# Optimization experiments

Hardware: AMD Instinct MI355X
Metric: run time of the kernel (lower is better)

The kernel has to match this reference:

```python
import jax, jax.numpy as jnp
import numpy as np

B, L, D = 4, 2048, 1024
DK, H = 64, 16
DFF = 4 * D
MASK_FILL = -2**15 + 1  # -32767, matches masked_fill value in source


def setup_inputs() -> dict:
    key = jax.random.key(0)
    ks = jax.random.split(key, 16)
    s = lambda fan_in: 1.0 / np.sqrt(fan_in)
    inp = {
        "x": jax.random.normal(ks[0], (B, L, D), dtype=jnp.float32),
        "maskPAD": jax.random.randint(ks[1], (B, L, L), 0, 2, dtype=jnp.int32),
        # attention projections (torch Linear layout: [out, in])
        "WQ_w": jax.random.uniform(ks[2], (H * DK, D), jnp.float32, -s(D), s(D)),
        "WQ_b": jnp.zeros((H * DK,), jnp.float32),
        "WK_w": jax.random.uniform(ks[3], (H * DK, D), jnp.float32, -s(D), s(D)),
        "WK_b": jnp.zeros((H * DK,), jnp.float32),
        "WV_w": jax.random.uniform(ks[4], (H * DK, D), jnp.float32, -s(D), s(D)),
        "WV_b": jnp.zeros((H * DK,), jnp.float32),
        "WO_w": jax.random.uniform(ks[5], (D, H * DK), jnp.float32, -s(H * DK), s(H * DK)),
        "WO_b": jnp.zeros((D,), jnp.float32),
        # FFN (pre-LN inside the FFN block)
        "ln_g": jnp.ones((D,), jnp.float32),
        "ln_b": jnp.zeros((D,), jnp.float32),
        "W1_w": jax.random.uniform(ks[6], (DFF, D), jnp.float32, -s(D), s(D)),
        "W1_b": jnp.zeros((DFF,), jnp.float32),
        "W2_w": jax.random.uniform(ks[7], (D, DFF), jnp.float32, -s(DFF), s(DFF)),
        "W2_b": jnp.zeros((D,), jnp.float32),
    }
    return inp


def _layernorm(x, g, b, eps=1e-5):
    mu = jnp.mean(x, axis=-1, keepdims=True)
    var = jnp.var(x, axis=-1, keepdims=True)
    return (x - mu) * jax.lax.rsqrt(var + eps) * g + b


def reference(x, maskPAD, WQ_w, WQ_b, WK_w, WK_b, WV_w, WV_b, WO_w, WO_b,
              ln_g, ln_b, W1_w, W1_b, W2_w, W2_b):
    # --- SelfAttention_PostLN (dropout = identity at eval) ---
    q = (jnp.einsum('bld,ed->ble', x, WQ_w) + WQ_b).reshape(B, L, H, DK).transpose(0, 2, 1, 3)
    k = (jnp.einsum('bld,ed->ble', x, WK_w) + WK_b).reshape(B, L, H, DK).transpose(0, 2, 1, 3)
    v = (jnp.einsum('bld,ed->ble', x, WV_w) + WV_b).reshape(B, L, H, DK).transpose(0, 2, 1, 3)
    scores = jnp.einsum('bhqd,bhkd->bhqk', q, k) / np.sqrt(DK).astype(np.float32)
    scores = jnp.where((maskPAD == 0)[:, None, :, :], jnp.float32(MASK_FILL), scores)
    alpha = jax.nn.softmax(scores, axis=-1)
    z = jnp.einsum('bhqk,bhkd->bhqd', alpha, v)  # [B,H,L,DK]
    z = z.transpose(0, 2, 1, 3).reshape(B, L, H * DK)
    z = jnp.einsum('ble,de->bld', z, WO_w) + WO_b
    # --- FFN_PreLN ---
    r = x + z                                    # residual 1 (dropout identity)
    h = _layernorm(r, ln_g, ln_b)
    h = jax.nn.relu(jnp.einsum('bld,fd->blf', h, W1_w) + W1_b)
    h = jnp.einsum('blf,df->bld', h, W2_w) + W2_b
    return r + h
```

## Files before the change

### kernel.cpp

```cpp
#include <hip/hip_runtime.h>

#define BD      4
#define LSEQ    2048
#define DMODEL  1024
#define HHEADS  16
#define DKK     64
#define DFFN    4096
#define MROWS   (BD*LSEQ)
#define QKVS    3072

typedef float  f32x4  __attribute__((ext_vector_type(4)));
typedef float  f32x16 __attribute__((ext_vector_type(16)));
typedef __bf16 bf16x8 __attribute__((ext_vector_type(8)));
typedef unsigned short u16x8 __attribute__((ext_vector_type(8)));
typedef unsigned int   u32x4 __attribute__((ext_vector_type(4)));

__device__ inline unsigned short f2bf(float x) {
    union { float f; unsigned u; } c; c.f = x;
    unsigned r = c.u + 0x7FFFu + ((c.u >> 16) & 1u);
    return (unsigned short)(r >> 16);
}

__global__ void cast_bf16_k(const float* __restrict__ in,
                            unsigned short* __restrict__ out, long n) {
    long i = ((long)blockIdx.x * blockDim.x + threadIdx.x) * 4;
    long stride = (long)gridDim.x * blockDim.x * 4;
    for (; i < n; i += stride) {
        float4 v = *(const float4*)(in + i);
        ushort4 o;
        o.x = f2bf(v.x); o.y = f2bf(v.y); o.z = f2bf(v.z); o.w = f2bf(v.w);
        *(ushort4*)(out + i) = o;
    }
}

__global__ __launch_bounds__(256) void maskbits_k(const int* __restrict__ m,
                                                  unsigned long long* __restrict__ bits) {
    const long gw = ((long)blockIdx.x * blockDim.x + threadIdx.x) >> 6;
    const int lane = threadIdx.x & 63;
    const int b   = (int)(gw >> 16);
    const int rem = (int)gw & 65535;
    const int q = rem >> 5, kt = rem & 31;
    const int v = m[((size_t)(b*LSEQ + q))*LSEQ + kt*64 + lane];
    const unsigned long long bal = __ballot(v != 0);
    if (lane == 0) bits[((size_t)(b*32 + kt))*LSEQ + q] = bal;
}

__device__ inline void gload16(const void* g, void* l) {
    __builtin_amdgcn_global_load_lds(
        (const __attribute__((address_space(1))) void*)g,
        (__attribute__((address_space(3))) void*)l, 16, 0, 0);
}

#define BAR() { __builtin_amdgcn_sched_barrier(0); __builtin_amdgcn_s_barrier(); __builtin_amdgcn_sched_barrier(0); }

#define STAGE(XSEL, XPTR, h, tau, s)                                              \
  { const unsigned short* gs0 = (XPTR) + (size_t)((h)*128 + wid*8 + srow) * K + (tau)*64 + schk*8; \
    gload16(gs0, (void*)&sm[(s)][(XSEL)][(((h)*128 + wid*8)*64)]);                 \
    gload16(gs0 + (size_t)64*K, (void*)&sm[(s)][(XSEL)][(((h)*128 + 64 + wid*8)*64)]); }

#define LDA(dst, s, mi, kk) dst = *(const bf16x8*)(&sm[(s)][0][(wr*128 + (mi)*16 + r0)*64 + ((((kk)*4 + g) ^ (r0 & 7)) << 3)]);
#define LDB(dst, s, nj, kk) dst = *(const bf16x8*)(&sm[(s)][1][(wc*64  + (nj)*16 + r0)*64 + ((((kk)*4 + g) ^ (r0 & 7)) << 3)]);

#define PHASE_MFMA(q)                                                                                   \
    __builtin_amdgcn_s_setprio(1);                                                                      \
    _Pragma("unroll")                                                                                   \
    for (int nj = 0; nj < 4; ++nj) {                                                                    \
        acc[2*(q)][nj]   = __builtin_amdgcn_mfma_f32_16x16x32_bf16(af00, bq[nj][0], acc[2*(q)][nj],   0,0,0); \
        acc[2*(q)][nj]   = __builtin_amdgcn_mfma_f32_16x16x32_bf16(af01, bq[nj][1], acc[2*(q)][nj],   0,0,0); \
        acc[2*(q)+1][nj] = __builtin_amdgcn_mfma_f32_16x16x32_bf16(af10, bq[nj][0], acc[2*(q)+1][nj], 0,0,0); \
        acc[2*(q)+1][nj] = __builtin_amdgcn_mfma_f32_16x16x32_bf16(af11, bq[nj][1], acc[2*(q)+1][nj], 0,0,0); \
    }                                                                                                   \
    __builtin_amdgcn_s_setprio(0);

#define KTILE(s, tau)                                                        \
  {                                                                          \
    const int tp1 = (tau) + 1, tp2 = (tau) + 2;                              \
    bf16x8 bq[4][2];                                                         \
    bf16x8 af00, af01, af10, af11;                                           \
                              \
    _Pragma("unroll") for (int nj = 0; nj < 4; ++nj) {                       \
        LDB(bq[nj][0], s, nj, 0); LDB(bq[nj][1], s, nj, 1); }                \
    LDA(af00, s, 0, 0); LDA(af01, s, 0, 1);                                  \
    LDA(af10, s, 1, 0); LDA(af11, s, 1, 1);                                  \
    if (tp1 < NTT) { STAGE(0, Ab, 0, tp1, (s)^1); }                          \
    BAR(); PHASE_MFMA(0); BAR();                                             \
                           \
    LDA(af00, s, 2, 0); LDA(af01, s, 2, 1);                                  \
    LDA(af10, s, 3, 0); LDA(af11, s, 3, 1);                                  \
    if (tp1 < NTT) { STAGE(0, Ab, 1, tp1, (s)^1); }                          \
    if (tp2 < NTT) { STAGE(1, Bb, 0, tp2, (s)); }                            \
    BAR(); PHASE_MFMA(1); BAR();                                             \
                                      \
    LDA(af00, s, 4, 0); LDA(af01, s, 4, 1);                                  \
    LDA(af10, s, 5, 0); LDA(af11, s, 5, 1);                                  \
    if (tp2 < NTT) { STAGE(1, Bb, 1, tp2, (s)); }                            \
    BAR(); PHASE_MFMA(2); BAR();                                             \
                                        \
    LDA(af00, s, 6, 0); LDA(af01, s, 6, 1);                                  \
    LDA(af10, s, 7, 0); LDA(af11, s, 7, 1);                                  \
    if (tp2 < NTT)      { asm volatile("s_waitcnt vmcnt(4)" ::: "memory"); } \
    else if (tp1 < NTT) { asm volatile("s_waitcnt vmcnt(0)" ::: "memory"); } \
    BAR(); PHASE_MFMA(3); BAR();                                             \
  }

template<int MODE, int NTT>
__global__ __launch_bounds__(512, 2) void gemm8(const unsigned short* __restrict__ A,
                                                const unsigned short* __restrict__ B,
                                                const float* __restrict__ bias,
                                                unsigned short* __restrict__ Cout,
                                                int M, int N, int K, float scaleQ)
{
    __shared__ unsigned short sm[2][2][256*64];
    const int t   = threadIdx.x;
    const int wid = t >> 6, lane = t & 63;
    const int wr  = wid >> 2, wc = wid & 3;
    const int r0  = lane & 15, g = lane >> 4;

    const int nwg = gridDim.x;
    const int bid = (blockIdx.x & 7) * (nwg >> 3) + (blockIdx.x >> 3);
    const int ntn = N >> 8;
    const int bm  = (bid / ntn) << 8, bn = (bid % ntn) << 8;

    const int srow = lane >> 3;
    const int schk = (lane & 7) ^ srow;
    const unsigned short* Ab = A + (size_t)bm * K;
    const unsigned short* Bb = B + (size_t)bn * K;

    f32x4 acc[8][4] = {};

    STAGE(1, Bb, 0, 0, 0); STAGE(1, Bb, 1, 0, 0);
    STAGE(0, Ab, 0, 0, 0); STAGE(0, Ab, 1, 0, 0);
    STAGE(1, Bb, 0, 1, 1); STAGE(1, Bb, 1, 1, 1);
    asm volatile("s_waitcnt vmcnt(4)" ::: "memory");
    BAR();

#pragma unroll 1
    for (int i2 = 0; i2 < NTT/2; ++i2) {
        const int tau = 2*i2;
        KTILE(0, tau);
        KTILE(1, tau+1);
    }

#pragma unroll
    for (int mi = 0; mi < 8; ++mi) {
        const int row0 = bm + wr*128 + mi*16 + g*4;
#pragma unroll
        for (int nj = 0; nj < 4; ++nj) {
            const int col = bn + wc*64 + nj*16 + r0;
            const float bcol = bias[col];
            const float sc = (MODE == 0) ? (col < 1024 ? scaleQ : 1.0f) : 1.0f;
#pragma unroll
            for (int rr = 0; rr < 4; ++rr) {
                float c = (acc[mi][nj][rr] + bcol) * sc;
                if (MODE == 1) c = fmaxf(c, 0.f);
                Cout[(size_t)(row0 + rr) * N + col] = f2bf(c);
            }
        }
    }
}

template<int MODE>
__global__ __launch_bounds__(256) void gemm_nt(const unsigned short* __restrict__ A,
                                               const unsigned short* __restrict__ B,
                                               const float* __restrict__ bias,
                                               const float* __restrict__ resid,
                                               void* __restrict__ Cout,
                                               int M, int N, int K, float scale)
{
    __shared__ unsigned short As[128*32];
    __shared__ unsigned short Bs[128*32];
    const int t    = threadIdx.x;
    const int w    = t >> 6, lane = t & 63;
    const int r0   = lane & 15, g = lane >> 4;
    const int wm   = (w >> 1) * 64, wn = (w & 1) * 64;
    const int bm   = blockIdx.y * 128, bn = blockIdx.x * 128;
    const int srow = t >> 2, scol = (t & 3) * 8;

    const unsigned short* Ag = A + (size_t)(bm + srow) * K + scol;
    const unsigned short* Bg = B + (size_t)(bn + srow) * K + scol;
    unsigned short* AsW = As + w * 512;
    unsigned short* BsW = Bs + w * 512;

    f32x4 acc[4][4] = {};

    for (int kt = 0; kt < K; kt += 32) {
        gload16(Ag + kt,                AsW);
        gload16(Ag + (size_t)64*K + kt, AsW + 2048);
        gload16(Bg + kt,                BsW);
        gload16(Bg + (size_t)64*K + kt, BsW + 2048);
        __syncthreads();
        bf16x8 af[4], bfr[4];
#pragma unroll
        for (int i = 0; i < 4; ++i)
            af[i] = *(const bf16x8*)(As + (wm + i*16 + r0)*32 + g*8);
#pragma unroll
        for (int j = 0; j < 4; ++j)
            bfr[j] = *(const bf16x8*)(Bs + (wn + j*16 + r0)*32 + g*8);
#pragma unroll
        for (int i = 0; i < 4; ++i)
#pragma unroll
            for (int j = 0; j < 4; ++j)
                acc[i][j] = __builtin_amdgcn_mfma_f32_16x16x32_bf16(af[i], bfr[j], acc[i][j], 0, 0, 0);
        __syncthreads();
    }

#pragma unroll
    for (int i = 0; i < 4; ++i) {
        const int row0 = bm + wm + i*16 + g*4;
#pragma unroll
        for (int j = 0; j < 4; ++j) {
            const int col = bn + wn + j*16 + r0;
            const float bcol = bias[col];
#pragma unroll
            for (int rr = 0; rr < 4; ++rr) {
                const int row = row0 + rr;
                float c = (acc[i][j][rr] + bcol) * scale;
                if (MODE == 2) {
                    ((float*)Cout)[(size_t)row * N + col] = c + resid[(size_t)row * N + col];
                } else {
                    if (MODE == 1) c = fmaxf(c, 0.f);
                    ((unsigned short*)Cout)[(size_t)row * N + col] = f2bf(c);
                }
            }
        }
    }
}

#define MFILL   (-47272.79f)
#define DEFTHR  (11.5415603f)
__global__ __launch_bounds__(256) void attn_k(
    const unsigned short* __restrict__ QKV,
    const unsigned long long* __restrict__ MBits,
    unsigned short* __restrict__ Z)
{
    __shared__ unsigned short Ks[2][64*64];
    __shared__ unsigned short Vt[64*64];
    __shared__ float Sc[4*32];

    const int t    = threadIdx.x;
    const int w    = t >> 6, lane = t & 63;
    const int q31  = lane & 31, hi = lane >> 5;

    const int bid = blockIdx.x;
    const int sw  = (bid & 7) * 128 + (bid >> 3);
    const int qt  = sw & 15, h = (sw >> 4) & 15, b = sw >> 8;
    const int qw  = qt * 128 + w * 32;

    const unsigned short* Qg = QKV + ((size_t)(b*LSEQ + qw + q31))*QKVS + h*DKK + hi*8;
    bf16x8 qf[4];
#pragma unroll
    for (int ds = 0; ds < 4; ++ds)
        qf[ds] = *(const bf16x8*)(Qg + ds*16);

    const int krow  = w*8 + (lane>>3);
    const int kchk  = (lane & 7) ^ (krow & 7);
    const unsigned short* Kg = QKV + ((size_t)(b*LSEQ))*QKVS + 1024 + h*DKK;
    const int kp   = w*8 + (lane>>3);
    const int vd0  = (lane & 7) * 8;
    const unsigned short* Vg = QKV + ((size_t)(b*LSEQ))*QKVS + 2048 + h*DKK + vd0;

    float m_r = MFILL, l_r = 0.f;
    f32x16 z0, z1;
#pragma unroll
    for (int r = 0; r < 16; ++r) { z0[r] = 0.f; z1[r] = 0.f; }

    u16x8 vA = *(const u16x8*)(Vg + (size_t)(kp*2)*QKVS);
    u16x8 vB = *(const u16x8*)(Vg + (size_t)(kp*2+1)*QKVS);
#pragma unroll
    for (int i = 0; i < 8; ++i) {
        const int d = vd0 + i;
        const int c = (kp>>2) ^ (d&7) ^ (d>>3);
        *(unsigned*)&Vt[d*64 + c*8 + 2*(kp&3)] = (unsigned)vA[i] | ((unsigned)vB[i] << 16);
    }
    gload16(Kg + (size_t)krow*QKVS      + kchk*8, &Ks[0][w*512]);
    gload16(Kg + (size_t)(32+krow)*QKVS + kchk*8, &Ks[0][w*512] + 2048);

    for (int kt = 0; kt < LSEQ/64; ++kt) {
        const int cur = kt & 1;
        __syncthreads();

        if (kt < LSEQ/64 - 1) {
            const int k0n = (kt+1)*64;
            gload16(Kg + (size_t)(k0n + krow)*QKVS      + kchk*8, &Ks[cur^1][w*512]);
            gload16(Kg + (size_t)(k0n + 32 + krow)*QKVS + kchk*8, &Ks[cur^1][w*512] + 2048);
            vA = *(const u16x8*)(Vg + (size_t)(k0n + kp*2)*QKVS);
            vB = *(const u16x8*)(Vg + (size_t)(k0n + kp*2+1)*QKVS);
        }
        const unsigned long long mw = MBits[((size_t)(b*32 + kt))*LSEQ + (qw + q31)];
        const unsigned long long sh = mw >> (hi*4);
        const unsigned md0 = (unsigned)sh, md1 = (unsigned)(sh >> 32);

        f32x16 s0, s1;
#pragma unroll
        for (int r = 0; r < 16; ++r) { s0[r] = 0.f; s1[r] = 0.f; }
        __builtin_amdgcn_s_setprio(1);
#pragma unroll
        for (int ds = 0; ds < 4; ++ds) {
            const int slot = ((ds*2 + hi) ^ (q31 & 7)) << 3;
            bf16x8 kf0 = *(const bf16x8*)(&Ks[cur][ q31     *64 + slot]);
            bf16x8 kf1 = *(const bf16x8*)(&Ks[cur][(32+q31)*64 + slot]);
            s0 = __builtin_amdgcn_mfma_f32_32x32x16_bf16(kf0, qf[ds], s0, 0, 0, 0);
            s1 = __builtin_amdgcn_mfma_f32_32x32x16_bf16(kf1, qf[ds], s1, 0, 0, 0);
        }
        __builtin_amdgcn_s_setprio(0);

#pragma unroll
        for (int r = 0; r < 16; ++r) {
            const int kb = (r & 3) + 8*(r >> 2);
            if (!((md0 >> kb) & 1)) s0[r] = MFILL;
            if (!((md1 >> kb) & 1)) s1[r] = MFILL;
        }

        float tm = fmaxf(s0[0], s1[0]);
#pragma unroll
        for (int r = 1; r < 16; ++r) tm = fmaxf(tm, fmaxf(s0[r], s1[r]));
        {
            float ta = tm, tb = tm;
            asm volatile("v_permlane32_swap_b32 %0, %1" : "+v"(ta), "+v"(tb));
            tm = fmaxf(tm, hi ? ta : tb);
        }

        if (__any(tm > m_r + DEFTHR)) {
            const float nm   = fmaxf(m_r, tm);
            const float corr = exp2f(m_r - nm);
            Sc[w*32 + q31] = corr;
            l_r *= corr;
            m_r  = nm;
#pragma unroll
            for (int r = 0; r < 16; ++r) {
                const int row = (r & 3) + 8*(r >> 2) + 4*hi;
                const float cr = Sc[w*32 + row];
                z0[r] *= cr; z1[r] *= cr;
            }
        }

#pragma unroll
        for (int r = 0; r < 16; ++r) {
            s0[r] = exp2f(s0[r] - m_r);
            s1[r] = exp2f(s1[r] - m_r);
        }
        float r4[8];
#pragma unroll
        for (int r = 0; r < 8; ++r)
            r4[r] = (s0[2*r] + s0[2*r+1]) + (s1[2*r] + s1[2*r+1]);
        float rs = ((r4[0]+r4[1]) + (r4[2]+r4[3])) + ((r4[4]+r4[5]) + (r4[6]+r4[7]));
        {
            float ra = rs, rb = rs;
            asm volatile("v_permlane32_swap_b32 %0, %1" : "+v"(ra), "+v"(rb));
            rs += hi ? ra : rb;
        }
        l_r += rs;

        bf16x8 pa[4];
#pragma unroll
        for (int half = 0; half < 2; ++half) {
#pragma unroll
            for (int sub = 0; sub < 2; ++sub) {
                const int base = sub*8;
                unsigned wa, wb, wc, wd;
                float p0 = half ? s1[base+0] : s0[base+0];
                float p1 = half ? s1[base+1] : s0[base+1];
                float p2 = half ? s1[base+2] : s0[base+2];
                float p3 = half ? s1[base+3] : s0[base+3];
                float p4 = half ? s1[base+4] : s0[base+4];
                float p5 = half ? s1[base+5] : s0[base+5];
                float p6 = half ? s1[base+6] : s0[base+6];
                float p7 = half ? s1[base+7] : s0[base+7];
                asm("v_cvt_pk_bf16_f32 %0, %1, %2" : "=v"(wa) : "v"(p0), "v"(p1));
                asm("v_cvt_pk_bf16_f32 %0, %1, %2" : "=v"(wb) : "v"(p4), "v"(p5));
                asm("v_cvt_pk_bf16_f32 %0, %1, %2" : "=v"(wc) : "v"(p2), "v"(p3));
                asm("v_cvt_pk_bf16_f32 %0, %1, %2" : "=v"(wd) : "v"(p6), "v"(p7));
                asm volatile("v_permlane32_swap_b32 %0, %1" : "+v"(wa), "+v"(wb));
                asm volatile("v_permlane32_swap_b32 %0, %1" : "+v"(wc), "+v"(wd));
                u32x4 pu; pu[0] = wa; pu[1] = wc; pu[2] = wb; pu[3] = wd;
                pa[half*2 + sub] = __builtin_bit_cast(bf16x8, pu);
            }
        }

        __builtin_amdgcn_s_setprio(1);
#pragma unroll
        for (int ks = 0; ks < 4; ++ks) {
            const int ch = ks*2 + hi;
            bf16x8 vf0 = *(const bf16x8*)(&Vt[ q31     *64 + ((ch ^ (q31&7) ^ ( q31>>3)     ) << 3)]);
            bf16x8 vf1 = *(const bf16x8*)(&Vt[(32+q31)*64 + ((ch ^ (q31&7) ^ ((32+q31)>>3)) << 3)]);
            z0 = __builtin_amdgcn_mfma_f32_32x32x16_bf16(pa[ks], vf0, z0, 0, 0, 0);
            z1 = __builtin_amdgcn_mfma_f32_32x32x16_bf16(pa[ks], vf1, z1, 0, 0, 0);
        }
        __builtin_amdgcn_s_setprio(0);

        __syncthreads();

        if (kt < LSEQ/64 - 1) {
#pragma unroll
            for (int i = 0; i < 8; ++i) {
                const int d = vd0 + i;
                const int c = (kp>>2) ^ (d&7) ^ (d>>3);
                *(unsigned*)&Vt[d*64 + c*8 + 2*(kp&3)] = (unsigned)vA[i] | ((unsigned)vB[i] << 16);
            }
        }
    }

    Sc[w*32 + q31] = l_r;
    unsigned short* Zb = Z + ((size_t)(b*LSEQ + qw))*DMODEL + h*DKK + q31;
#pragma unroll
    for (int r = 0; r < 16; ++r) {
        const int row = (r & 3) + 8*(r >> 2) + 4*hi;
        const float rl = 1.0f / Sc[w*32 + row];
        Zb[(size_t)row*DMODEL]      = f2bf(z0[r] * rl);
        Zb[(size_t)row*DMODEL + 32] = f2bf(z1[r] * rl);
    }
}

__global__ __launch_bounds__(256) void ln_k(const float* __restrict__ r,
                                            const float* __restrict__ gam,
                                            const float* __restrict__ bet,
                                            unsigned short* __restrict__ out)
{
    const int row = blockIdx.x;
    const int t = threadIdx.x;
    const float* rp = r + (size_t)row * DMODEL;
    float4 v = *(const float4*)(rp + t*4);
    float s  = v.x + v.y + v.z + v.w;
    float s2 = v.x*v.x + v.y*v.y + v.z*v.z + v.w*v.w;
#pragma unroll
    for (int off = 32; off >= 1; off >>= 1) {
        s  += __shfl_xor(s,  off);
        s2 += __shfl_xor(s2, off);
    }
    __shared__ float red[8];
    const int wv = t >> 6;
    if ((t & 63) == 0) { red[wv] = s; red[4 + wv] = s2; }
    __syncthreads();
    s  = red[0] + red[1] + red[2] + red[3];
    s2 = red[4] + red[5] + red[6] + red[7];
    const float mu   = s  * (1.f/DMODEL);
    const float var  = s2 * (1.f/DMODEL) - mu*mu;
    const float rstd = rsqrtf(var + 1e-5f);
    float4 gv = *(const float4*)(gam + t*4);
    float4 bv = *(const float4*)(bet + t*4);
    ushort4 o;
    o.x = f2bf((v.x - mu)*rstd*gv.x + bv.x);
    o.y = f2bf((v.y - mu)*rstd*gv.y + bv.y);
    o.z = f2bf((v.z - mu)*rstd*gv.z + bv.z);
    o.w = f2bf((v.w - mu)*rstd*gv.w + bv.w);
    *(ushort4*)(out + (size_t)row * DMODEL + t*4) = o;
}

extern "C" void kernel_launch(void* const* d_in, const int* in_sizes, int n_in,
                              void* d_out, int out_size, void* d_ws, size_t ws_size,
                              hipStream_t stream)
{
    const float* x    = (const float*)d_in[0];
    const int*   mask = (const int*)  d_in[1];
    const float* WQ_w = (const float*)d_in[2];
    const float* WQ_b = (const float*)d_in[3];
    const float* WK_w = (const float*)d_in[4];
    const float* WK_b = (const float*)d_in[5];
    const float* WV_w = (const float*)d_in[6];
    const float* WV_b = (const float*)d_in[7];
    const float* WO_w = (const float*)d_in[8];
    const float* WO_b = (const float*)d_in[9];
    const float* ln_g = (const float*)d_in[10];
    const float* ln_b = (const float*)d_in[11];
    const float* W1_w = (const float*)d_in[12];
    const float* W1_b = (const float*)d_in[13];
    const float* W2_w = (const float*)d_in[14];
    const float* W2_b = (const float*)d_in[15];
    float* out = (float*)d_out;

    char* w = (char*)d_ws;
    const size_t MB = 1024*1024;
    unsigned short* qkv  = (unsigned short*)(w + 0*MB);
    unsigned short* Zb   = (unsigned short*)(w + 48*MB);
    unsigned short* xb   = (unsigned short*)(w + 64*MB);
    float*          rb   = (float*)         (w + 80*MB);
    unsigned short* wqkv = (unsigned short*)(w + 112*MB);
    unsigned short* wob  = (unsigned short*)(w + 118*MB);
    unsigned short* w1b  = (unsigned short*)(w + 120*MB);
    unsigned short* w2b  = (unsigned short*)(w + 128*MB);
    unsigned long long* mbits = (unsigned long long*)(w + 136*MB);
    float* bqkv = (float*)(w + 48*MB);
    unsigned short* hln  = xb;
    unsigned short* hmid = (unsigned short*)(w + 0*MB);

    cast_bf16_k<<<2048, 256, 0, stream>>>(x,    xb,   (long)MROWS*DMODEL);
    cast_bf16_k<<<512,  256, 0, stream>>>(WQ_w, wqkv,                 (long)DMODEL*DMODEL);
    cast_bf16_k<<<512,  256, 0, stream>>>(WK_w, wqkv + 1024*1024,     (long)DMODEL*DMODEL);
    cast_bf16_k<<<512,  256, 0, stream>>>(WV_w, wqkv + 2*1024*1024,   (long)DMODEL*DMODEL);
    cast_bf16_k<<<512,  256, 0, stream>>>(WO_w, wob,  (long)DMODEL*DMODEL);
    cast_bf16_k<<<2048, 256, 0, stream>>>(W1_w, w1b,  (long)DFFN*DMODEL);
    cast_bf16_k<<<2048, 256, 0, stream>>>(W2_w, w2b,  (long)DMODEL*DFFN);
    maskbits_k<<<65536, 256, 0, stream>>>(mask, mbits);
    hipMemcpyAsync(bqkv,        WQ_b, 1024*sizeof(float), hipMemcpyDeviceToDevice, stream);
    hipMemcpyAsync(bqkv + 1024, WK_b, 1024*sizeof(float), hipMemcpyDeviceToDevice, stream);
    hipMemcpyAsync(bqkv + 2048, WV_b, 1024*sizeof(float), hipMemcpyDeviceToDevice, stream);

    gemm8<0, 16><<<dim3(384), dim3(512), 0, stream>>>(xb, wqkv, bqkv, qkv,
                                                      MROWS, QKVS, DMODEL, 0.18033688f);
    attn_k<<<dim3(1024), dim3(256), 0, stream>>>(qkv, mbits, Zb);
    gemm_nt<2><<<dim3(8, 64), dim3(256), 0, stream>>>(Zb, wob, WO_b, x, rb, MROWS, DMODEL, DMODEL, 1.0f);
    ln_k<<<MROWS, 256, 0, stream>>>(rb, ln_g, ln_b, hln);
    gemm8<1, 16><<<dim3(512), dim3(512), 0, stream>>>(hln, w1b, W1_b, hmid,
                                                      MROWS, DFFN, DMODEL, 1.0f);
    gemm_nt<2><<<dim3(8, 64), dim3(256), 0, stream>>>(hmid, w2b, W2_b, rb, out, MROWS, DMODEL, DFFN, 1.0f);
}
```

Baseline: 519.4 us.

## Add 256x128 GEMM variant, restructure attention pipelining, fuse bias concat

```diff
diff --git a/kernel.cpp b/kernel.cpp
--- a/kernel.cpp
+++ b/kernel.cpp
@@ -31,6 +31,12 @@
         o.x = f2bf(v.x); o.y = f2bf(v.y); o.z = f2bf(v.z); o.w = f2bf(v.w);
         *(ushort4*)(out + i) = o;
     }
+}
+
+__global__ void concat3_k(const float* __restrict__ a, const float* __restrict__ b,
+                          const float* __restrict__ c, float* __restrict__ o) {
+    int i = blockIdx.x * 256 + threadIdx.x;
+    if (i < 1024) { o[i] = a[i]; o[1024 + i] = b[i]; o[2048 + i] = c[i]; }
 }
 
 __global__ __launch_bounds__(256) void maskbits_k(const int* __restrict__ m,
@@ -77,25 +83,21 @@
     const int tp1 = (tau) + 1, tp2 = (tau) + 2;                              \
     bf16x8 bq[4][2];                                                         \
     bf16x8 af00, af01, af10, af11;                                           \
-                              \
     _Pragma("unroll") for (int nj = 0; nj < 4; ++nj) {                       \
         LDB(bq[nj][0], s, nj, 0); LDB(bq[nj][1], s, nj, 1); }                \
     LDA(af00, s, 0, 0); LDA(af01, s, 0, 1);                                  \
     LDA(af10, s, 1, 0); LDA(af11, s, 1, 1);                                  \
     if (tp1 < NTT) { STAGE(0, Ab, 0, tp1, (s)^1); }                          \
     BAR(); PHASE_MFMA(0); BAR();                                             \
-                           \
     LDA(af00, s, 2, 0); LDA(af01, s, 2, 1);                                  \
     LDA(af10, s, 3, 0); LDA(af11, s, 3, 1);                                  \
     if (tp1 < NTT) { STAGE(0, Ab, 1, tp1, (s)^1); }                          \
     if (tp2 < NTT) { STAGE(1, Bb, 0, tp2, (s)); }                            \
     BAR(); PHASE_MFMA(1); BAR();                                             \
-                                      \
     LDA(af00, s, 4, 0); LDA(af01, s, 4, 1);                                  \
     LDA(af10, s, 5, 0); LDA(af11, s, 5, 1);                                  \
     if (tp2 < NTT) { STAGE(1, Bb, 1, tp2, (s)); }                            \
     BAR(); PHASE_MFMA(2); BAR();                                             \
-                                        \
     LDA(af00, s, 6, 0); LDA(af01, s, 6, 1);                                  \
     LDA(af10, s, 7, 0); LDA(af11, s, 7, 1);                                  \
     if (tp2 < NTT)      { asm volatile("s_waitcnt vmcnt(4)" ::: "memory"); } \
@@ -104,7 +106,7 @@
   }
 
 template<int MODE, int NTT>
-__global__ __launch_bounds__(512, 2) void gemm8(const unsigned short* __restrict__ A,
+__global__ __launch_bounds__(512, 1) void gemm8(const unsigned short* __restrict__ A,
                                                 const unsigned short* __restrict__ B,
                                                 const float* __restrict__ bias,
                                                 unsigned short* __restrict__ Cout,
@@ -154,6 +156,118 @@
                 float c = (acc[mi][nj][rr] + bcol) * sc;
                 if (MODE == 1) c = fmaxf(c, 0.f);
                 Cout[(size_t)(row0 + rr) * N + col] = f2bf(c);
+            }
+        }
+    }
+}
+
+#define STAGEA2(h, tau, s)                                                        \
+  { const unsigned short* gs0 = Ab + (size_t)((h)*128 + wid*8 + srow) * K + (tau)*64 + schk*8; \
+    gload16(gs0, (void*)&smA[(s)][(((h)*128 + wid*8)*64)]);                        \
+    gload16(gs0 + (size_t)64*K, (void*)&smA[(s)][(((h)*128 + 64 + wid*8)*64)]); }
+
+#define STAGEB2(tau, s)                                                           \
+  { const unsigned short* gs0 = Bb + (size_t)(wid*8 + srow) * K + (tau)*64 + schk*8; \
+    gload16(gs0, (void*)&smB[(s)][((wid*8)*64)]);                                  \
+    gload16(gs0 + (size_t)64*K, (void*)&smB[(s)][((64 + wid*8)*64)]); }
+
+#define LDA2(dst, s, mi, kk) dst = *(const bf16x8*)(&smA[(s)][(wr*128 + (mi)*16 + r0)*64 + ((((kk)*4 + g) ^ (r0 & 7)) << 3)]);
+#define LDB2(dst, s, nj, kk) dst = *(const bf16x8*)(&smB[(s)][(wc*32  + (nj)*16 + r0)*64 + ((((kk)*4 + g) ^ (r0 & 7)) << 3)]);
+
+#define PHASE_MFMA2(q)                                                                                  \
+    __builtin_amdgcn_s_setprio(1);                                                                      \
+    _Pragma("unroll")                                                                                   \
+    for (int nj = 0; nj < 2; ++nj) {                                                                    \
+        acc[2*(q)][nj]   = __builtin_amdgcn_mfma_f32_16x16x32_bf16(af00, bq[nj][0], acc[2*(q)][nj],   0,0,0); \
+        acc[2*(q)][nj]   = __builtin_amdgcn_mfma_f32_16x16x32_bf16(af01, bq[nj][1], acc[2*(q)][nj],   0,0,0); \
+        acc[2*(q)+1][nj] = __builtin_amdgcn_mfma_f32_16x16x32_bf16(af10, bq[nj][0], acc[2*(q)+1][nj], 0,0,0); \
+        acc[2*(q)+1][nj] = __builtin_amdgcn_mfma_f32_16x16x32_bf16(af11, bq[nj][1], acc[2*(q)+1][nj], 0,0,0); \
+    }                                                                                                   \
+    __builtin_amdgcn_s_setprio(0);
+
+#define KTILE2(s, tau)                                                       \
+  {                                                                          \
+    const int tp1 = (tau) + 1, tp2 = (tau) + 2;                              \
+    bf16x8 bq[2][2];                                                         \
+    bf16x8 af00, af01, af10, af11;                                           \
+    _Pragma("unroll") for (int nj = 0; nj < 2; ++nj) {                       \
+        LDB2(bq[nj][0], s, nj, 0); LDB2(bq[nj][1], s, nj, 1); }              \
+    LDA2(af00, s, 0, 0); LDA2(af01, s, 0, 1);                                \
+    LDA2(af10, s, 1, 0); LDA2(af11, s, 1, 1);                                \
+    if (tp1 < NTT) { STAGEA2(0, tp1, (s)^1); }                               \
+    BAR(); PHASE_MFMA2(0); BAR();                                            \
+    LDA2(af00, s, 2, 0); LDA2(af01, s, 2, 1);                                \
+    LDA2(af10, s, 3, 0); LDA2(af11, s, 3, 1);                                \
+    if (tp1 < NTT) { STAGEA2(1, tp1, (s)^1); }                               \
+    BAR(); PHASE_MFMA2(1); BAR();                                            \
+    LDA2(af00, s, 4, 0); LDA2(af01, s, 4, 1);                                \
+    LDA2(af10, s, 5, 0); LDA2(af11, s, 5, 1);                                \
+    if (tp2 < NTT) { STAGEB2(tp2, (s)); }                                    \
+    BAR(); PHASE_MFMA2(2); BAR();                                            \
+    LDA2(af00, s, 6, 0); LDA2(af01, s, 6, 1);                                \
+    LDA2(af10, s, 7, 0); LDA2(af11, s, 7, 1);                                \
+    if (tp2 < NTT)      { asm volatile("s_waitcnt vmcnt(2)" ::: "memory"); } \
+    else if (tp1 < NTT) { asm volatile("s_waitcnt vmcnt(0)" ::: "memory"); } \
+    BAR(); PHASE_MFMA2(3); BAR();                                            \
+  }
+
+template<int MODE, int NTT>
+__global__ __launch_bounds__(512, 1) void gemm8n(const unsigned short* __restrict__ A,
+                                                 const unsigned short* __restrict__ B,
+                                                 const float* __restrict__ bias,
+                                                 const float* __restrict__ resid,
+                                                 void* __restrict__ Cout,
+                                                 int M, int N, int K, float scaleQ)
+{
+    __shared__ unsigned short smA[2][256*64];
+    __shared__ unsigned short smB[2][128*64];
+    const int t   = threadIdx.x;
+    const int wid = t >> 6, lane = t & 63;
+    const int wr  = wid >> 2, wc = wid & 3;
+    const int r0  = lane & 15, g = lane >> 4;
+
+    const int nwg = gridDim.x;
+    const int bid = (blockIdx.x & 7) * (nwg >> 3) + (blockIdx.x >> 3);
+    const int ntn = N >> 7;
+    const int bm  = (bid / ntn) << 8, bn = (bid % ntn) << 7;
+
+    const int srow = lane >> 3;
+    const int schk = (lane & 7) ^ srow;
+    const unsigned short* Ab = A + (size_t)bm * K;
+    const unsigned short* Bb = B + (size_t)bn * K;
+
+    f32x4 acc[8][2] = {};
+
+    STAGEB2(0, 0);
+    STAGEA2(0, 0, 0); STAGEA2(1, 0, 0);
+    STAGEB2(1, 1);
+    asm volatile("s_waitcnt vmcnt(2)" ::: "memory");
+    BAR();
+
+#pragma unroll 1
+    for (int i2 = 0; i2 < NTT/2; ++i2) {
+        const int tau = 2*i2;
+        KTILE2(0, tau);
+        KTILE2(1, tau+1);
+    }
+
+#pragma unroll
+    for (int mi = 0; mi < 8; ++mi) {
+        const int row0 = bm + wr*128 + mi*16 + g*4;
+#pragma unroll
+        for (int nj = 0; nj < 2; ++nj) {
+            const int col = bn + wc*32 + nj*16 + r0;
+            const float bcol = bias[col];
+            const float sc = (MODE == 0) ? (col < 1024 ? scaleQ : 1.0f) : 1.0f;
+#pragma unroll
+            for (int rr = 0; rr < 4; ++rr) {
+                const int row = row0 + rr;
+                float c = (acc[mi][nj][rr] + bcol) * sc;
+                if (MODE == 2) {
+                    ((float*)Cout)[(size_t)row * N + col] = c + resid[(size_t)row * N + col];
+                } else {
+                    ((unsigned short*)Cout)[(size_t)row * N + col] = f2bf(c);
+                }
             }
         }
     }
@@ -234,7 +348,8 @@
     unsigned short* __restrict__ Z)
 {
     __shared__ unsigned short Ks[2][64*64];
-    __shared__ unsigned short Vt[64*64];
+    __shared__ unsigned short Vt[2][64*64];
+    __shared__ unsigned short Qs[128*64];
     __shared__ float Sc[4*32];
 
     const int t    = threadIdx.x;
@@ -246,11 +361,16 @@
     const int qt  = sw & 15, h = (sw >> 4) & 15, b = sw >> 8;
     const int qw  = qt * 128 + w * 32;
 
-    const unsigned short* Qg = QKV + ((size_t)(b*LSEQ + qw + q31))*QKVS + h*DKK + hi*8;
-    bf16x8 qf[4];
-#pragma unroll
-    for (int ds = 0; ds < 4; ++ds)
-        qf[ds] = *(const bf16x8*)(Qg + ds*16);
+    {
+        const int qrow = t & 127;
+        const int cb   = (t >> 7) * 4;
+        const unsigned short* Qgs = QKV + ((size_t)(b*LSEQ + qt*128 + qrow))*QKVS + h*DKK;
+#pragma unroll
+        for (int j = 0; j < 4; ++j) {
+            u16x8 qv = *(const u16x8*)(Qgs + (cb + j)*8);
+            *(u16x8*)&Qs[qrow*64 + (((cb + j) ^ (qrow & 7)) << 3)] = qv;
+        }
+    }
 
     const int krow  = w*8 + (lane>>3);
     const int kchk  = (lane & 7) ^ (krow & 7);
@@ -258,35 +378,40 @@
     const int kp   = w*8 + (lane>>3);
     const int vd0  = (lane & 7) * 8;
     const unsigned short* Vg = QKV + ((size_t)(b*LSEQ))*QKVS + 2048 + h*DKK + vd0;
+    const unsigned short* Qrow = &Qs[(w*32 + q31)*64];
 
     float m_r = MFILL, l_r = 0.f;
     f32x16 z0, z1;
 #pragma unroll
     for (int r = 0; r < 16; ++r) { z0[r] = 0.f; z1[r] = 0.f; }
 
-    u16x8 vA = *(const u16x8*)(Vg + (size_t)(kp*2)*QKVS);
-    u16x8 vB = *(const u16x8*)(Vg + (size_t)(kp*2+1)*QKVS);
-#pragma unroll
-    for (int i = 0; i < 8; ++i) {
-        const int d = vd0 + i;
-        const int c = (kp>>2) ^ (d&7) ^ (d>>3);
-        *(unsigned*)&Vt[d*64 + c*8 + 2*(kp&3)] = (unsigned)vA[i] | ((unsigned)vB[i] << 16);
+    {
+        u16x8 vA = *(const u16x8*)(Vg + (size_t)(kp*2)*QKVS);
+        u16x8 vB = *(const u16x8*)(Vg + (size_t)(kp*2+1)*QKVS);
+#pragma unroll
+        for (int i = 0; i < 8; ++i) {
+            const int d = vd0 + i;
+            const int c = (kp>>2) ^ (d&7) ^ (d>>3);
+            *(unsigned*)&Vt[0][d*64 + c*8 + 2*(kp&3)] = (unsigned)vA[i] | ((unsigned)vB[i] << 16);
+        }
     }
     gload16(Kg + (size_t)krow*QKVS      + kchk*8, &Ks[0][w*512]);
     gload16(Kg + (size_t)(32+krow)*QKVS + kchk*8, &Ks[0][w*512] + 2048);
+    unsigned long long mw = MBits[((size_t)(b*32 + 0))*LSEQ + (qw + q31)];
+
+    __syncthreads();
 
     for (int kt = 0; kt < LSEQ/64; ++kt) {
         const int cur = kt & 1;
-        __syncthreads();
-
-        if (kt < LSEQ/64 - 1) {
-            const int k0n = (kt+1)*64;
-            gload16(Kg + (size_t)(k0n + krow)*QKVS      + kchk*8, &Ks[cur^1][w*512]);
-            gload16(Kg + (size_t)(k0n + 32 + krow)*QKVS + kchk*8, &Ks[cur^1][w*512] + 2048);
-            vA = *(const u16x8*)(Vg + (size_t)(k0n + kp*2)*QKVS);
-            vB = *(const u16x8*)(Vg + (size_t)(k0n + kp*2+1)*QKVS);
-        }
-        const unsigned long long mw = MBits[((size_t)(b*32 + kt))*LSEQ + (qw + q31)];
+        const int ktn = (kt < LSEQ/64 - 1) ? kt + 1 : kt;
+        const int k0n = ktn * 64;
+
+        gload16(Kg + (size_t)(k0n + krow)*QKVS      + kchk*8, &Ks[cur^1][w*512]);
+        gload16(Kg + (size_t)(k0n + 32 + krow)*QKVS + kchk*8, &Ks[cur^1][w*512] + 2048);
+        u16x8 vA = *(const u16x8*)(Vg + (size_t)(k0n + kp*2)*QKVS);
+        u16x8 vB = *(const u16x8*)(Vg + (size_t)(k0n + kp*2+1)*QKVS);
+        const unsigned long long mwn = MBits[((size_t)(b*32 + ktn))*LSEQ + (qw + q31)];
+
         const unsigned long long sh = mw >> (hi*4);
         const unsigned md0 = (unsigned)sh, md1 = (unsigned)(sh >> 32);
 
@@ -299,8 +424,9 @@
             const int slot = ((ds*2 + hi) ^ (q31 & 7)) << 3;
             bf16x8 kf0 = *(const bf16x8*)(&Ks[cur][ q31     *64 + slot]);
             bf16x8 kf1 = *(const bf16x8*)(&Ks[cur][(32+q31)*64 + slot]);
-            s0 = __builtin_amdgcn_mfma_f32_32x32x16_bf16(kf0, qf[ds], s0, 0, 0, 0);
-            s1 = __builtin_amdgcn_mfma_f32_32x32x16_bf16(kf1, qf[ds], s1, 0, 0, 0);
+            bf16x8 qf  = *(const bf16x8*)(Qrow + slot);
+            s0 = __builtin_amdgcn_mfma_f32_32x32x16_bf16(kf0, qf, s0, 0, 0, 0);
+            s1 = __builtin_amdgcn_mfma_f32_32x32x16_bf16(kf1, qf, s1, 0, 0, 0);
         }
         __builtin_amdgcn_s_setprio(0);
 
@@ -351,13 +477,13 @@
         }
         l_r += rs;
 
-        bf16x8 pa[4];
+        __builtin_amdgcn_s_setprio(1);
 #pragma unroll
         for (int half = 0; half < 2; ++half) {
 #pragma unroll
             for (int sub = 0; sub < 2; ++sub) {
                 const int base = sub*8;
-                unsigned wa, wb, wc, wd;
+                unsigned wa, wb, wc2, wd;
                 float p0 = half ? s1[base+0] : s0[base+0];
                 float p1 = half ? s1[base+1] : s0[base+1];
                 float p2 = half ? s1[base+2] : s0[base+2];
@@ -368,36 +494,30 @@
                 float p7 = half ? s1[base+7] : s0[base+7];
                 asm("v_cvt_pk_bf16_f32 %0, %1, %2" : "=v"(wa) : "v"(p0), "v"(p1));
                 asm("v_cvt_pk_bf16_f32 %0, %1, %2" : "=v"(wb) : "v"(p4), "v"(p5));
-                asm("v_cvt_pk_bf16_f32 %0, %1, %2" : "=v"(wc) : "v"(p2), "v"(p3));
+                asm("v_cvt_pk_bf16_f32 %0, %1, %2" : "=v"(wc2) : "v"(p2), "v"(p3));
                 asm("v_cvt_pk_bf16_f32 %0, %1, %2" : "=v"(wd) : "v"(p6), "v"(p7));
                 asm volatile("v_permlane32_swap_b32 %0, %1" : "+v"(wa), "+v"(wb));
-                asm volatile("v_permlane32_swap_b32 %0, %1" : "+v"(wc), "+v"(wd));
-                u32x4 pu; pu[0] = wa; pu[1] = wc; pu[2] = wb; pu[3] = wd;
-                pa[half*2 + sub] = __builtin_bit_cast(bf16x8, pu);
+                asm volatile("v_permlane32_swap_b32 %0, %1" : "+v"(wc2), "+v"(wd));
+                u32x4 pu; pu[0] = wa; pu[1] = wc2; pu[2] = wb; pu[3] = wd;
+                bf16x8 pa = __builtin_bit_cast(bf16x8, pu);
+                const int ks = half*2 + sub;
+                const int ch = ks*2 + hi;
+                bf16x8 vf0 = *(const bf16x8*)(&Vt[cur][ q31     *64 + ((ch ^ (q31&7) ^ ( q31>>3)     ) << 3)]);
+                bf16x8 vf1 = *(const bf16x8*)(&Vt[cur][(32+q31)*64 + ((ch ^ (q31&7) ^ ((32+q31)>>3)) << 3)]);
+                z0 = __builtin_amdgcn_mfma_f32_32x32x16_bf16(pa, vf0, z0, 0, 0, 0);
+                z1 = __builtin_amdgcn_mfma_f32_32x32x16_bf16(pa, vf1, z1, 0, 0, 0);
             }
         }
-
-        __builtin_amdgcn_s_setprio(1);
-#pragma unroll
-        for (int ks = 0; ks < 4; ++ks) {
-            const int ch = ks*2 + hi;
-            bf16x8 vf0 = *(const bf16x8*)(&Vt[ q31     *64 + ((ch ^ (q31&7) ^ ( q31>>3)     ) << 3)]);
-            bf16x8 vf1 = *(const bf16x8*)(&Vt[(32+q31)*64 + ((ch ^ (q31&7) ^ ((32+q31)>>3)) << 3)]);
-            z0 = __builtin_amdgcn_mfma_f32_32x32x16_bf16(pa[ks], vf0, z0, 0, 0, 0);
-            z1 = __builtin_amdgcn_mfma_f32_32x32x16_bf16(pa[ks], vf1, z1, 0, 0, 0);
-        }
         __builtin_amdgcn_s_setprio(0);
 
+#pragma unroll
+        for (int i = 0; i < 8; ++i) {
+            const int d = vd0 + i;
+            const int c = (kp>>2) ^ (d&7) ^ (d>>3);
+            *(unsigned*)&Vt[cur^1][d*64 + c*8 + 2*(kp&3)] = (unsigned)vA[i] | ((unsigned)vB[i] << 16);
+        }
+        mw = mwn;
         __syncthreads();
-
-        if (kt < LSEQ/64 - 1) {
-#pragma unroll
-            for (int i = 0; i < 8; ++i) {
-                const int d = vd0 + i;
-                const int c = (kp>>2) ^ (d&7) ^ (d>>3);
-                *(unsigned*)&Vt[d*64 + c*8 + 2*(kp&3)] = (unsigned)vA[i] | ((unsigned)vB[i] << 16);
-            }
-        }
     }
 
     Sc[w*32 + q31] = l_r;
@@ -484,23 +604,22 @@
     unsigned short* hmid = (unsigned short*)(w + 0*MB);
 
     cast_bf16_k<<<2048, 256, 0, stream>>>(x,    xb,   (long)MROWS*DMODEL);
-    cast_bf16_k<<<512,  256, 0, stream>>>(WQ_w, wqkv,                 (long)DMODEL*DMODEL);
-    cast_bf16_k<<<512,  256, 0, stream>>>(WK_w, wqkv + 1024*1024,     (long)DMODEL*DMODEL);
-    cast_bf16_k<<<512,  256, 0, stream>>>(WV_w, wqkv + 2*1024*1024,   (long)DMODEL*DMODEL);
+    cast_bf16_k<<<512,  256, 0, stream>>>(WQ_w, wqkv,               (long)DMODEL*DMODEL);
+    cast_bf16_k<<<512,  256, 0, stream>>>(WK_w, wqkv + 1024*1024,   (long)DMODEL*DMODEL);
+    cast_bf16_k<<<512,  256, 0, stream>>>(WV_w, wqkv + 2*1024*1024, (long)DMODEL*DMODEL);
     cast_bf16_k<<<512,  256, 0, stream>>>(WO_w, wob,  (long)DMODEL*DMODEL);
     cast_bf16_k<<<2048, 256, 0, stream>>>(W1_w, w1b,  (long)DFFN*DMODEL);
     cast_bf16_k<<<2048, 256, 0, stream>>>(W2_w, w2b,  (long)DMODEL*DFFN);
     maskbits_k<<<65536, 256, 0, stream>>>(mask, mbits);
-    hipMemcpyAsync(bqkv,        WQ_b, 1024*sizeof(float), hipMemcpyDeviceToDevice, stream);
-    hipMemcpyAsync(bqkv + 1024, WK_b, 1024*sizeof(float), hipMemcpyDeviceToDevice, stream);
-    hipMemcpyAsync(bqkv + 2048, WV_b, 1024*sizeof(float), hipMemcpyDeviceToDevice, stream);
-
-    gemm8<0, 16><<<dim3(384), dim3(512), 0, stream>>>(xb, wqkv, bqkv, qkv,
-                                                      MROWS, QKVS, DMODEL, 0.18033688f);
+    concat3_k<<<4, 256, 0, stream>>>(WQ_b, WK_b, WV_b, bqkv);
+
+    gemm8n<0, 16><<<dim3(768), dim3(512), 0, stream>>>(xb, wqkv, bqkv, nullptr, qkv,
+                                                       MROWS, QKVS, DMODEL, 0.18033688f);
     attn_k<<<dim3(1024), dim3(256), 0, stream>>>(qkv, mbits, Zb);
     gemm_nt<2><<<dim3(8, 64), dim3(256), 0, stream>>>(Zb, wob, WO_b, x, rb, MROWS, DMODEL, DMODEL, 1.0f);
     ln_k<<<MROWS, 256, 0, stream>>>(rb, ln_g, ln_b, hln);
     gemm8<1, 16><<<dim3(512), dim3(512), 0, stream>>>(hln, w1b, W1_b, hmid,
                                                       MROWS, DFFN, DMODEL, 1.0f);
-    gemm_nt<2><<<dim3(8, 64), dim3(256), 0, stream>>>(hmid, w2b, W2_b, rb, out, MROWS, DMODEL, DFFN, 1.0f);
-}
+    gemm8n<2, 64><<<dim3(256), dim3(512), 0, stream>>>(hmid, w2b, W2_b, rb, out,
+                                                       MROWS, DMODEL, DFFN, 1.0f);
+}
```

After: 508.2 us. 1.02x faster.
